# Kernel tuning notes

Hardware: AMD Instinct MI355X
Metric: run time of the kernel (lower is better)

Reference implementation:

```python
import jax, jax.numpy as jnp
import numpy as np

T = 2048          # tokens (single-sequence prefill)
HID = 4096        # hidden_size
NH = 32           # num attention heads
NKV = 8           # num kv heads (GQA)
HD = 128          # head_dim
QKV_OUT = (NH + 2 * NKV) * HD  # 6144
THETA = 10000.0
SCALING = HD ** -0.5


def setup_inputs() -> dict:
    key = jax.random.key(0)
    ks = jax.random.split(key, 8)
    positions = jnp.arange(T, dtype=jnp.int32)
    # per-token int8 quantized hidden states (symmetric, [-127,127])
    q_act = jax.random.randint(ks[0], (T, HID), -127, 128, dtype=jnp.int32)
    # per-token dynamic activation scale
    act_scale = jax.random.uniform(ks[1], (T,), jnp.float32) * 0.01 + 0.001
    # int4 weights stored unsigned [0,15] with per-output-channel scale & zero point
    w_qkv_q = jax.random.randint(ks[2], (QKV_OUT, HID), 0, 16, dtype=jnp.int32)
    w_qkv_scale = jax.random.uniform(ks[3], (QKV_OUT,), jnp.float32) * 0.01 + 0.001
    w_qkv_zero = jax.random.uniform(ks[4], (QKV_OUT,), jnp.float32) * 2.0 + 7.0
    w_o_q = jax.random.randint(ks[5], (HID, HID), 0, 16, dtype=jnp.int32)
    w_o_scale = jax.random.uniform(ks[6], (HID,), jnp.float32) * 0.01 + 0.001
    w_o_zero = jax.random.uniform(ks[7], (HID,), jnp.float32) * 2.0 + 7.0
    return dict(positions=positions, q_act=q_act, act_scale=act_scale,
                w_qkv_q=w_qkv_q, w_qkv_scale=w_qkv_scale, w_qkv_zero=w_qkv_zero,
                w_o_q=w_o_q, w_o_scale=w_o_scale, w_o_zero=w_o_zero)


def w4a8_linear(qa_f, s_a, a_sum, qw, s_w, z_w):
    # y[t,o] = s_a[t]*s_w[o] * ( (qa @ qw^T)[t,o] - z_w[o]*sum_j qa[t,j] )
    acc = jnp.matmul(qa_f, qw.astype(jnp.float32).T)  # [T, O]
    return (s_a[:, None] * s_w[None, :]) * (acc - z_w[None, :] * a_sum[:, None])


def apply_rope(x, positions):
    # neox-style RoPE over full head_dim
    half = HD // 2
    inv_freq = THETA ** (-jnp.arange(0, half, dtype=jnp.float32) / half * 1.0)
    inv_freq = 1.0 / (THETA ** (jnp.arange(0, HD, 2, dtype=jnp.float32) / HD))
    freqs = positions.astype(jnp.float32)[:, None] * inv_freq[None, :]  # [T, HD/2]
    cos = jnp.cos(freqs)[:, None, :]
    sin = jnp.sin(freqs)[:, None, :]
    x1, x2 = x[..., :half], x[..., half:]
    return jnp.concatenate([x1 * cos - x2 * sin, x2 * cos + x1 * sin], axis=-1)


def dynamic_quant_with_sum(x):
    # per-token symmetric int8 dynamic quantization + fused sum
    s = jnp.maximum(jnp.max(jnp.abs(x), axis=-1), 1e-8) / 127.0  # [T]
    q = jnp.clip(jnp.round(x / s[:, None]), -127, 127)
    return q, s, jnp.sum(q, axis=-1)


def reference(positions, q_act, act_scale, w_qkv_q, w_qkv_scale, w_qkv_zero,
              w_o_q, w_o_scale, w_o_zero):
    qa_f = q_act.astype(jnp.float32)
    a_sum = jnp.sum(qa_f, axis=-1)  # fused activation sum
    qkv = w4a8_linear(qa_f, act_scale, a_sum, w_qkv_q, w_qkv_scale, w_qkv_zero)
    q, k, v = jnp.split(qkv, [NH * HD, NH * HD + NKV * HD], axis=-1)
    q = q.reshape(T, NH, HD)
    k = k.reshape(T, NKV, HD)
    v = v.reshape(T, NKV, HD)
    q = apply_rope(q, positions)
    k = apply_rope(k, positions)
    # GQA: repeat kv heads
    rep = NH // NKV
    k = jnp.repeat(k, rep, axis=1)  # [T, NH, HD]
    v = jnp.repeat(v, rep, axis=1)
    scores = jnp.einsum('qhd,khd->hqk', q, k) * SCALING  # [NH, T, T]
    causal = jnp.tril(jnp.ones((T, T), dtype=bool))
    scores = jnp.where(causal[None], scores, -jnp.inf)
    probs = jax.nn.softmax(scores, axis=-1)
    attn = jnp.einsum('hqk,khd->qhd', probs, v).reshape(T, NH * HD)
    # invoke_quant_fuse_sum: dynamic per-token quantization of attn output
    q2, s2, sum2 = dynamic_quant_with_sum(attn)
    out = w4a8_linear(q2, s2, sum2, w_o_q, w_o_scale, w_o_zero)
    return out
```

## Files before the change

### kernel.cpp

```cpp
#include <hip/hip_runtime.h>

#define T 2048
#define HID 4096
#define NH 32
#define NKV 8
#define HD 128
#define QKV_OUT ((NH + 2*NKV) * HD)
#define SCALING 0.08838834764831843f
#define ROPE_C 0.20762050593046014f

typedef __attribute__((ext_vector_type(8))) short bfrag;
typedef __attribute__((ext_vector_type(4))) float ffrag;
typedef __attribute__((ext_vector_type(4))) int  ifrag;
typedef __attribute__((ext_vector_type(16))) char c16;

__device__ __forceinline__ short f2bf(float f) {
  unsigned u = __builtin_bit_cast(unsigned, f);
  u += 0x7fffu + ((u >> 16) & 1u);
  return (short)(u >> 16);
}

__device__ __forceinline__ void split2(float x, short& hi, short& lo) {
  unsigned u = __builtin_bit_cast(unsigned, x);
  unsigned uh = u + (0x7fffu + ((u >> 16) & 1u));
  hi = (short)(uh >> 16);
  float fh = __builtin_bit_cast(float, uh & 0xffff0000u);
  float r = x - fh;
  unsigned ur = __builtin_bit_cast(unsigned, r);
  ur += 0x7fffu + ((ur >> 16) & 1u);
  lo = (short)(ur >> 16);
}

__device__ __forceinline__ void gload_lds16(const void* g, void* l) {
  __builtin_amdgcn_global_load_lds(
      (const __attribute__((address_space(1))) unsigned int*)g,
      (__attribute__((address_space(3))) unsigned int*)l, 16, 0, 0);
}

__global__ __launch_bounds__(256)
void asum_conv(const int* __restrict__ qact, float* __restrict__ a_sum,
               char* __restrict__ a_i8) {
  __shared__ int red[256];
  const int t = blockIdx.x, tid = threadIdx.x;
  const int* row = qact + (size_t)t * HID + tid * 16;
  int s = 0;
  c16 o;
#pragma unroll
  for (int i = 0; i < 4; i++) {
    int4 v = *(const int4*)(row + i * 4);
    s += v.x + v.y + v.z + v.w;
    o[i*4+0] = (char)v.x; o[i*4+1] = (char)v.y;
    o[i*4+2] = (char)v.z; o[i*4+3] = (char)v.w;
  }
  *(c16*)(a_i8 + (size_t)t * HID + tid * 16) = o;
  red[tid] = s; __syncthreads();
  for (int off = 128; off > 0; off >>= 1) {
    if (tid < off) red[tid] += red[tid + off];
    __syncthreads();
  }
  if (tid == 0) a_sum[t] = (float)red[0];
}

__global__ __launch_bounds__(256)
void conv_i2c(const int* __restrict__ src, char* __restrict__ dst, int n16) {
  int idx = blockIdx.x * 256 + threadIdx.x;
  if (idx >= n16) return;
  const int4* s4 = (const int4*)src + (size_t)idx * 4;
  c16 o;
#pragma unroll
  for (int j = 0; j < 4; j++) {
    int4 v = s4[j];
    o[j*4+0] = (char)v.x; o[j*4+1] = (char)v.y;
    o[j*4+2] = (char)v.z; o[j*4+3] = (char)v.w;
  }
  *(c16*)(dst + (size_t)idx * 16) = o;
}

__global__ __launch_bounds__(256)
void gemm_i8(const char* __restrict__ A, const char* __restrict__ W,
             const float* __restrict__ s_a, const float* __restrict__ asum,
             const float* __restrict__ s_w, const float* __restrict__ z_w,
             float* __restrict__ C, int M, int N, int K) {
  __shared__ __align__(16) char As[128 * 64];
  __shared__ __align__(16) char Bs[128 * 64];
  const int tid = threadIdx.x;
  const int lane = tid & 63;
  const int quad = lane >> 4, l15 = lane & 15;
  const int wave = tid >> 6;
  const int wm = (wave >> 1) * 64, wn = (wave & 1) * 64;
  const int bm = blockIdx.y * 128, bn = blockIdx.x * 128;
  const int sr = tid >> 2, sc = (tid & 3) * 16;

  ifrag acc[4][4];
#pragma unroll
  for (int mi = 0; mi < 4; mi++)
#pragma unroll
    for (int ni = 0; ni < 4; ni++)
      acc[mi][ni] = (ifrag){0, 0, 0, 0};

  for (int k0 = 0; k0 < K; k0 += 64) {
#pragma unroll
    for (int it = 0; it < 2; it++) {
      gload_lds16(A + (size_t)(bm + it * 64 + sr) * K + k0 + sc,
                  &As[it * 4096 + wave * 1024]);
      gload_lds16(W + (size_t)(bn + it * 64 + sr) * K + k0 + sc,
                  &Bs[it * 4096 + wave * 1024]);
    }
    __syncthreads();

    ifrag af[4], bfv[4];
#pragma unroll
    for (int mi = 0; mi < 4; mi++)
      af[mi] = *(const ifrag*)&As[(wm + mi * 16 + l15) * 64 + quad * 16];
#pragma unroll
    for (int ni = 0; ni < 4; ni++)
      bfv[ni] = *(const ifrag*)&Bs[(wn + ni * 16 + l15) * 64 + quad * 16];
#pragma unroll
    for (int mi = 0; mi < 4; mi++)
#pragma unroll
      for (int ni = 0; ni < 4; ni++)
        acc[mi][ni] = __builtin_amdgcn_mfma_i32_16x16x64_i8(
            af[mi], bfv[ni], acc[mi][ni], 0, 0, 0);
    __syncthreads();
  }

#pragma unroll
  for (int mi = 0; mi < 4; mi++) {
    int row0 = bm + wm + mi * 16 + quad * 4;
#pragma unroll
    for (int r = 0; r < 4; r++) {
      int row = row0 + r;
      float sa = s_a[row], av = asum[row];
#pragma unroll
      for (int ni = 0; ni < 4; ni++) {
        int col = bn + wn + ni * 16 + l15;
        C[(size_t)row * N + col] = (sa * s_w[col]) * ((float)acc[mi][ni][r] - z_w[col] * av);
      }
    }
  }
}

__global__ __launch_bounds__(256)
void split_kv(float* __restrict__ qkv, const int* __restrict__ positions,
              short* __restrict__ Kh, short* __restrict__ Kl,
              short* __restrict__ Vth) {
  __shared__ __align__(16) short Vh_lds[128 * 72];
  const int y = blockIdx.y;
  const int t0 = blockIdx.x * 64;
  const int tid = threadIdx.x;

  if (y >= NKV) {
    const int h = y - NKV;
#pragma unroll
    for (int it = 0; it < 4; it++) {
      int c = tid + 256 * it;
      int key = c >> 4, dc = c & 15;
      float* qr = qkv + (size_t)(t0 + key) * QKV_OUT + (size_t)h * HD;
      float4 a = *(const float4*)(qr + dc * 4);
      float4 b = *(const float4*)(qr + dc * 4 + 64);
      float av[4] = {a.x, a.y, a.z, a.w};
      float bv[4] = {b.x, b.y, b.z, b.w};
      float pos = (float)positions[t0 + key];
#pragma unroll
      for (int jj = 0; jj < 4; jj++) {
        float fr = pos * exp2f(-ROPE_C * (float)(dc * 4 + jj));
        float sn, cs; sincosf(fr, &sn, &cs);
        float x1 = av[jj], x2 = bv[jj];
        av[jj] = x1 * cs - x2 * sn;
        bv[jj] = x2 * cs + x1 * sn;
      }
      *(float4*)(qr + dc * 4)      = make_float4(av[0], av[1], av[2], av[3]);
      *(float4*)(qr + dc * 4 + 64) = make_float4(bv[0], bv[1], bv[2], bv[3]);
    }
    return;
  }

  const int kvh = y;
#pragma unroll
  for (int it = 0; it < 4; it++) {
    int c = tid + 256 * it;
    int key = c >> 4, dc = c & 15;
    const float* kr = qkv + (size_t)(t0 + key) * QKV_OUT
                      + (size_t)NH * HD + (size_t)kvh * HD;
    float4 a = *(const float4*)(kr + dc * 4);
    float4 b = *(const float4*)(kr + dc * 4 + 64);
    float av[4] = {a.x, a.y, a.z, a.w};
    float bv[4] = {b.x, b.y, b.z, b.w};
    float pos = (float)positions[t0 + key];
    short4 ha, la, hb, lb;
    short hh, ll;
#pragma unroll
    for (int jj = 0; jj < 4; jj++) {
      float fr = pos * exp2f(-ROPE_C * (float)(dc * 4 + jj));
      float sn, cs; sincosf(fr, &sn, &cs);
      float x1 = av[jj], x2 = bv[jj];
      float r1 = x1 * cs - x2 * sn;
      float r2 = x2 * cs + x1 * sn;
      split2(r1, hh, ll); ((short*)&ha)[jj] = hh; ((short*)&la)[jj] = ll;
      split2(r2, hh, ll); ((short*)&hb)[jj] = hh; ((short*)&lb)[jj] = ll;
    }
    size_t o1 = (size_t)kvh * T * HD + (size_t)(t0 + key) * HD + dc * 4;
    *(short4*)(Kh + o1) = ha;      *(short4*)(Kl + o1) = la;
    *(short4*)(Kh + o1 + 64) = hb; *(short4*)(Kl + o1 + 64) = lb;
  }
#pragma unroll
  for (int i = 0; i < 8; i++) {
    int c = tid + 256 * i;
    int key = c >> 5, dc = c & 31;
    float4 f = *(const float4*)(qkv + (size_t)(t0 + key) * QKV_OUT
                                + (size_t)(NH + NKV) * HD + (size_t)kvh * HD + dc * 4);
    Vh_lds[(dc*4+0)*72 + key] = f2bf(f.x);
    Vh_lds[(dc*4+1)*72 + key] = f2bf(f.y);
    Vh_lds[(dc*4+2)*72 + key] = f2bf(f.z);
    Vh_lds[(dc*4+3)*72 + key] = f2bf(f.w);
  }
  __syncthreads();
#pragma unroll
  for (int i = 0; i < 2; i++) {
    int c = tid + 256 * i;
    int row = c >> 2, cc = c & 3;
    size_t o = (size_t)kvh * HD * T + (size_t)row * T + t0 + cc * 8;
    *(bfrag*)(Vth + o) = *(const bfrag*)&Vh_lds[row * 72 + cc * 8];
  }
#pragma unroll
  for (int i = 0; i < 2; i++) {
    int c = tid + 256 * i;
    int row = c >> 2, cc = c & 3;
    size_t o = (size_t)kvh * HD * T + (size_t)row * T + t0 + 32 + cc * 8;
    *(bfrag*)(Vth + o) = *(const bfrag*)&Vh_lds[row * 72 + 32 + cc * 8];
  }
}

__global__ __launch_bounds__(256)
void attn_kernel(const float* __restrict__ qkv,
                 const short* __restrict__ Kh, const short* __restrict__ Kl,
                 const short* __restrict__ Vth,
                 float* __restrict__ attn) {
  __shared__ __align__(16) short Ksh[32 * 136];
  __shared__ __align__(16) short Ksl[32 * 136];
  __shared__ __align__(16) short Vsh[128 * 40];
  __shared__ __align__(16) short Psh[4 * 16 * 40];

  const int kvh = blockIdx.y;
  const int pair = blockIdx.x;
  const int tid = threadIdx.x;
  const int lane = tid & 63;
  const int wv = tid >> 6;
  const int l15 = lane & 15, quad = lane >> 4;
  const int h = kvh * 4 + wv;
  short* Pw = Psh + wv * 16 * 40;

  const short* KhB = Kh + (size_t)kvh * T * HD;
  const short* KlB = Kl + (size_t)kvh * T * HD;
  const short* VhB = Vth + (size_t)kvh * HD * T;

  const int kr = tid >> 4, kc8 = (tid & 15) * 8;
  const int vd = tid >> 2, vc8 = (tid & 3) * 8;

  bfrag rkh0, rkh1, rkl0, rkl1, rv0, rv1;
  auto preload = [&](int k0) {
    rkh0 = *(const bfrag*)(KhB + (size_t)(k0 + kr) * HD + kc8);
    rkh1 = *(const bfrag*)(KhB + (size_t)(k0 + kr + 16) * HD + kc8);
    rkl0 = *(const bfrag*)(KlB + (size_t)(k0 + kr) * HD + kc8);
    rkl1 = *(const bfrag*)(KlB + (size_t)(k0 + kr + 16) * HD + kc8);
    rv0  = *(const bfrag*)(VhB + (size_t)vd * T + k0 + vc8);
    rv1  = *(const bfrag*)(VhB + (size_t)(vd + 64) * T + k0 + vc8);
  };
  preload(0);

  bfrag ones;
#pragma unroll
  for (int j = 0; j < 8; j++) ones[j] = (short)0x3f80;

  for (int pass = 0; pass < 2; pass++) {
    const int qt = pass ? pair : 127 - pair;
    const int q0 = qt * 16;
    const int nk = (q0 >> 5) + 1;

    bfrag qh[4], ql[4];
    const float* qrow = qkv + (size_t)(q0 + l15) * QKV_OUT + (size_t)h * HD;
#pragma unroll
    for (int kc = 0; kc < 4; kc++) {
      float4 f0 = *(const float4*)(qrow + kc * 32 + quad * 8);
      float4 f1 = *(const float4*)(qrow + kc * 32 + quad * 8 + 4);
      float fv[8] = {f0.x, f0.y, f0.z, f0.w, f1.x, f1.y, f1.z, f1.w};
#pragma unroll
      for (int j = 0; j < 8; j++) {
        short hi, lo; split2(fv[j], hi, lo);
        qh[kc][j] = hi; ql[kc][j] = lo;
      }
    }

    ffrag o[8], ol;
    ol = (ffrag){0.f, 0.f, 0.f, 0.f};
#pragma unroll
    for (int n = 0; n < 8; n++) o[n] = (ffrag){0.f, 0.f, 0.f, 0.f};
    float m_i[4] = {-1e30f, -1e30f, -1e30f, -1e30f};

    for (int kt = 0; kt < nk; kt++) {
      const int k0 = kt << 5;
      __syncthreads();
      *(bfrag*)&Ksh[kr * 136 + kc8] = rkh0;
      *(bfrag*)&Ksh[(kr + 16) * 136 + kc8] = rkh1;
      *(bfrag*)&Ksl[kr * 136 + kc8] = rkl0;
      *(bfrag*)&Ksl[(kr + 16) * 136 + kc8] = rkl1;
      *(bfrag*)&Vsh[vd * 40 + vc8] = rv0;
      *(bfrag*)&Vsh[(vd + 64) * 40 + vc8] = rv1;
      if (kt + 1 < nk) preload(k0 + 32);
      else if (pass == 0) preload(0);
      __syncthreads();

      ffrag s[2];
      s[0] = (ffrag){0.f,0.f,0.f,0.f}; s[1] = (ffrag){0.f,0.f,0.f,0.f};
#pragma unroll
      for (int n = 0; n < 2; n++) {
#pragma unroll
        for (int kc = 0; kc < 4; kc++) {
          bfrag bh = *(const bfrag*)&Ksh[(n*16 + l15) * 136 + kc*32 + quad*8];
          bfrag bl = *(const bfrag*)&Ksl[(n*16 + l15) * 136 + kc*32 + quad*8];
          s[n] = __builtin_amdgcn_mfma_f32_16x16x32_bf16(qh[kc], bh, s[n], 0,0,0);
          s[n] = __builtin_amdgcn_mfma_f32_16x16x32_bf16(qh[kc], bl, s[n], 0,0,0);
          s[n] = __builtin_amdgcn_mfma_f32_16x16x32_bf16(ql[kc], bh, s[n], 0,0,0);
        }
      }
      const bool last = (kt == nk - 1);
      float sv[2][4];
#pragma unroll
      for (int n = 0; n < 2; n++)
#pragma unroll
        for (int r = 0; r < 4; r++) {
          float v = s[n][r] * SCALING;
          if (last) {
            int key = k0 + n * 16 + l15;
            int row = q0 + quad * 4 + r;
            if (key > row) v = -1e30f;
          }
          sv[n][r] = v;
        }
      float alpha[4];
      bool anyup = false;
#pragma unroll
      for (int r = 0; r < 4; r++) {
        float mt = fmaxf(sv[0][r], sv[1][r]);
        mt = fmaxf(mt, __shfl_xor(mt, 1));
        mt = fmaxf(mt, __shfl_xor(mt, 2));
        mt = fmaxf(mt, __shfl_xor(mt, 4));
        mt = fmaxf(mt, __shfl_xor(mt, 8));
        float m_new = fmaxf(m_i[r], mt);
        alpha[r] = __expf(m_i[r] - m_new);
        if (m_new > m_i[r]) anyup = true;
        m_i[r] = m_new;
      }
#pragma unroll
      for (int n = 0; n < 2; n++)
#pragma unroll
        for (int r = 0; r < 4; r++) {
          float p = __expf(sv[n][r] - m_i[r]);
          Pw[(quad*4 + r) * 40 + n*16 + l15] = f2bf(p);
        }
      if (__any(anyup)) {
#pragma unroll
        for (int r = 0; r < 4; r++) ol[r] *= alpha[r];
#pragma unroll
        for (int n = 0; n < 8; n++)
#pragma unroll
          for (int r = 0; r < 4; r++) o[n][r] *= alpha[r];
      }
      bfrag ph = *(const bfrag*)&Pw[l15 * 40 + quad * 8];
      ol = __builtin_amdgcn_mfma_f32_16x16x32_bf16(ph, ones, ol, 0,0,0);
#pragma unroll
      for (int n = 0; n < 8; n++) {
        bfrag vh = *(const bfrag*)&Vsh[(n*16 + l15) * 40 + quad * 8];
        o[n] = __builtin_amdgcn_mfma_f32_16x16x32_bf16(ph, vh, o[n], 0,0,0);
      }
    }

    float inv[4];
#pragma unroll
    for (int r = 0; r < 4; r++) inv[r] = 1.f / ol[r];
#pragma unroll
    for (int n = 0; n < 8; n++)
#pragma unroll
      for (int r = 0; r < 4; r++) {
        int row = q0 + quad * 4 + r;
        attn[(size_t)row * HID + (size_t)h * HD + n * 16 + l15] = o[n][r] * inv[r];
      }
  }
}

__global__ __launch_bounds__(256)
void quant_kernel(const float* __restrict__ x, char* __restrict__ q2,
                  float* __restrict__ s2, float* __restrict__ sum2) {
  __shared__ float red[256];
  const int t = blockIdx.x, tid = threadIdx.x;
  const float* row = x + (size_t)t * HID;
  float4 v[4];
  float m = 0.f;
#pragma unroll
  for (int i = 0; i < 4; i++) {
    v[i] = *(const float4*)(row + tid * 16 + i * 4);
    m = fmaxf(m, fmaxf(fmaxf(fabsf(v[i].x), fabsf(v[i].y)),
                       fmaxf(fabsf(v[i].z), fabsf(v[i].w))));
  }
  red[tid] = m; __syncthreads();
  for (int off = 128; off > 0; off >>= 1) {
    if (tid < off) red[tid] = fmaxf(red[tid], red[tid + off]);
    __syncthreads();
  }
  float s = fmaxf(red[0], 1e-8f) / 127.f;
  __syncthreads();
  float ssum = 0.f;
  c16 o;
#pragma unroll
  for (int i = 0; i < 4; i++) {
    float q;
    q = fminf(127.f, fmaxf(-127.f, rintf(v[i].x / s))); ssum += q; o[i*4+0] = (char)(int)q;
    q = fminf(127.f, fmaxf(-127.f, rintf(v[i].y / s))); ssum += q; o[i*4+1] = (char)(int)q;
    q = fminf(127.f, fmaxf(-127.f, rintf(v[i].z / s))); ssum += q; o[i*4+2] = (char)(int)q;
    q = fminf(127.f, fmaxf(-127.f, rintf(v[i].w / s))); ssum += q; o[i*4+3] = (char)(int)q;
  }
  *(c16*)(q2 + (size_t)t * HID + tid * 16) = o;
  red[tid] = ssum; __syncthreads();
  for (int off = 128; off > 0; off >>= 1) {
    if (tid < off) red[tid] += red[tid + off];
    __syncthreads();
  }
  if (tid == 0) { s2[t] = s; sum2[t] = red[0]; }
}

extern "C" void kernel_launch(void* const* d_in, const int* in_sizes, int n_in,
                              void* d_out, int out_size, void* d_ws, size_t ws_size,
                              hipStream_t stream) {
  const int*   positions   = (const int*)d_in[0];
  const int*   q_act       = (const int*)d_in[1];
  const float* act_scale   = (const float*)d_in[2];
  const int*   w_qkv_q     = (const int*)d_in[3];
  const float* w_qkv_scale = (const float*)d_in[4];
  const float* w_qkv_zero  = (const float*)d_in[5];
  const int*   w_o_q       = (const int*)d_in[6];
  const float* w_o_scale   = (const float*)d_in[7];
  const float* w_o_zero    = (const float*)d_in[8];
  float* out = (float*)d_out;

  size_t off = 0;
  auto alloc = [&](size_t bytes) -> void* {
    void* p = (char*)d_ws + off;
    off += (bytes + 255) & ~(size_t)255;
    return p;
  };
  float* qkv   = (float*)alloc((size_t)T * QKV_OUT * 4);
  char*  act8  = (char*)alloc((size_t)T * HID);
  short* Kh    = (short*)alloc((size_t)NKV * T * HD * 2);
  short* Kl    = (short*)alloc((size_t)NKV * T * HD * 2);
  short* Vth   = (short*)alloc((size_t)NKV * T * HD * 2);
  char*  w8    = (char*)alloc((size_t)QKV_OUT * HID);
  float* a_sum = (float*)alloc(T * 4);
  float* s2    = (float*)alloc(T * 4);
  float* sum2  = (float*)alloc(T * 4);
  (void)ws_size;

  asum_conv<<<T, 256, 0, stream>>>(q_act, a_sum, act8);
  conv_i2c<<<(QKV_OUT * HID / 16 + 255) / 256, 256, 0, stream>>>(
      w_qkv_q, w8, QKV_OUT * HID / 16);
  gemm_i8<<<dim3(QKV_OUT / 128, T / 128), 256, 0, stream>>>(
      act8, w8, act_scale, a_sum, w_qkv_scale, w_qkv_zero, qkv, T, QKV_OUT, HID);
  split_kv<<<dim3(T / 64, NKV + NH), 256, 0, stream>>>(qkv, positions, Kh, Kl, Vth);
  attn_kernel<<<dim3(64, NKV), 256, 0, stream>>>(qkv, Kh, Kl, Vth, out);
  conv_i2c<<<(HID * HID / 16 + 255) / 256, 256, 0, stream>>>(
      w_o_q, w8, HID * HID / 16);
  quant_kernel<<<T, 256, 0, stream>>>(out, act8, s2, sum2);
  gemm_i8<<<dim3(HID / 128, T / 128), 256, 0, stream>>>(
      act8, w8, s2, sum2, w_o_scale, w_o_zero, out, T, HID, HID);
}
```

Measured before the change: 535.2 us.

## Split attention KV range across two blocks and merge partials in a combine kernel

Each (query-tile pair, kv head) block is split into two blocks, one for even and one for odd 32-key tiles. This doubles the attention grid to improve CU occupancy and load balance. Each half writes unnormalised outputs plus its running max and sum. A new combine kernel rescales the two halves with log-sum-exp weights and writes the normalised result. The partial buffer reuses the act8/w8 workspace region, and launch bounds now request 4 waves per EU. The cost is an extra kernel launch and roughly two extra full passes over the fp32 attention output in memory.

Result: slower. 758.4 us (+41.7%).

```diff
diff --git a/kernel.cpp b/kernel.cpp
--- a/kernel.cpp
+++ b/kernel.cpp
@@ -231,18 +231,20 @@
   }
 }
 
-__global__ __launch_bounds__(256)
+__global__ __launch_bounds__(256, 4)
 void attn_kernel(const float* __restrict__ qkv,
                  const short* __restrict__ Kh, const short* __restrict__ Kl,
                  const short* __restrict__ Vth,
-                 float* __restrict__ attn) {
+                 float* __restrict__ Opart, float* __restrict__ Mp,
+                 float* __restrict__ Lp, float* __restrict__ attn) {
   __shared__ __align__(16) short Ksh[32 * 136];
   __shared__ __align__(16) short Ksl[32 * 136];
   __shared__ __align__(16) short Vsh[128 * 40];
   __shared__ __align__(16) short Psh[4 * 16 * 40];
 
   const int kvh = blockIdx.y;
-  const int pair = blockIdx.x;
+  const int pair = blockIdx.x >> 1;
+  const int half = blockIdx.x & 1;
   const int tid = threadIdx.x;
   const int lane = tid & 63;
   const int wv = tid >> 6;
@@ -266,7 +268,7 @@
     rv0  = *(const bfrag*)(VhB + (size_t)vd * T + k0 + vc8);
     rv1  = *(const bfrag*)(VhB + (size_t)(vd + 64) * T + k0 + vc8);
   };
-  preload(0);
+  preload(half * 32);
 
   bfrag ones;
 #pragma unroll
@@ -297,7 +299,7 @@
     for (int n = 0; n < 8; n++) o[n] = (ffrag){0.f, 0.f, 0.f, 0.f};
     float m_i[4] = {-1e30f, -1e30f, -1e30f, -1e30f};
 
-    for (int kt = 0; kt < nk; kt++) {
+    for (int kt = half; kt < nk; kt += 2) {
       const int k0 = kt << 5;
       __syncthreads();
       *(bfrag*)&Ksh[kr * 136 + kc8] = rkh0;
@@ -306,8 +308,8 @@
       *(bfrag*)&Ksl[(kr + 16) * 136 + kc8] = rkl1;
       *(bfrag*)&Vsh[vd * 40 + vc8] = rv0;
       *(bfrag*)&Vsh[(vd + 64) * 40 + vc8] = rv1;
-      if (kt + 1 < nk) preload(k0 + 32);
-      else if (pass == 0) preload(0);
+      if (kt + 2 < nk) preload(k0 + 64);
+      else if (pass == 0) preload(half * 32);
       __syncthreads();
 
       ffrag s[2];
@@ -375,16 +377,48 @@
       }
     }
 
-    float inv[4];
-#pragma unroll
-    for (int r = 0; r < 4; r++) inv[r] = 1.f / ol[r];
+    float* dst = half ? attn : Opart;
 #pragma unroll
     for (int n = 0; n < 8; n++)
 #pragma unroll
       for (int r = 0; r < 4; r++) {
         int row = q0 + quad * 4 + r;
-        attn[(size_t)row * HID + (size_t)h * HD + n * 16 + l15] = o[n][r] * inv[r];
-      }
+        dst[(size_t)row * HID + (size_t)h * HD + n * 16 + l15] = o[n][r];
+      }
+    if (l15 == 0) {
+#pragma unroll
+      for (int r = 0; r < 4; r++) {
+        int row = q0 + quad * 4 + r;
+        size_t ix = (size_t)half * NH * T + (size_t)h * T + row;
+        Mp[ix] = m_i[r];
+        Lp[ix] = ol[r];
+      }
+    }
+  }
+}
+
+__global__ __launch_bounds__(256)
+void attn_combine(const float* __restrict__ Opart, const float* __restrict__ Mp,
+                  const float* __restrict__ Lp, float* attn) {
+  const int row = blockIdx.x, tid = threadIdx.x;
+  const int h = tid >> 3;
+  const float m0 = Mp[(size_t)h * T + row];
+  const float m1 = Mp[(size_t)NH * T + (size_t)h * T + row];
+  const float l0 = Lp[(size_t)h * T + row];
+  const float l1 = Lp[(size_t)NH * T + (size_t)h * T + row];
+  const float m = fmaxf(m0, m1);
+  float s0 = __expf(m0 - m), s1 = __expf(m1 - m);
+  const float inv = 1.f / (l0 * s0 + l1 * s1);
+  s0 *= inv; s1 *= inv;
+  const size_t base = (size_t)row * HID + (size_t)tid * 16;
+  float4* dst = (float4*)(attn + base);
+  const float4* p0 = (const float4*)(Opart + base);
+#pragma unroll
+  for (int i = 0; i < 4; i++) {
+    float4 a = p0[i];
+    float4 b = dst[i];
+    dst[i] = make_float4(a.x * s0 + b.x * s1, a.y * s0 + b.y * s1,
+                         a.z * s0 + b.z * s1, a.w * s0 + b.w * s1);
   }
 }
 
@@ -450,13 +484,16 @@
   };
   float* qkv   = (float*)alloc((size_t)T * QKV_OUT * 4);
   char*  act8  = (char*)alloc((size_t)T * HID);
+  char*  w8    = (char*)alloc((size_t)QKV_OUT * HID);
   short* Kh    = (short*)alloc((size_t)NKV * T * HD * 2);
   short* Kl    = (short*)alloc((size_t)NKV * T * HD * 2);
   short* Vth   = (short*)alloc((size_t)NKV * T * HD * 2);
-  char*  w8    = (char*)alloc((size_t)QKV_OUT * HID);
   float* a_sum = (float*)alloc(T * 4);
   float* s2    = (float*)alloc(T * 4);
   float* sum2  = (float*)alloc(T * 4);
+  float* Mp    = (float*)alloc((size_t)2 * NH * T * 4);
+  float* Lp    = (float*)alloc((size_t)2 * NH * T * 4);
+  float* Opart = (float*)act8;
   (void)ws_size;
 
   asum_conv<<<T, 256, 0, stream>>>(q_act, a_sum, act8);
@@ -465,7 +502,9 @@
   gemm_i8<<<dim3(QKV_OUT / 128, T / 128), 256, 0, stream>>>(
       act8, w8, act_scale, a_sum, w_qkv_scale, w_qkv_zero, qkv, T, QKV_OUT, HID);
   split_kv<<<dim3(T / 64, NKV + NH), 256, 0, stream>>>(qkv, positions, Kh, Kl, Vth);
-  attn_kernel<<<dim3(64, NKV), 256, 0, stream>>>(qkv, Kh, Kl, Vth, out);
+  attn_kernel<<<dim3(128, NKV), 256, 0, stream>>>(
+      qkv, Kh, Kl, Vth, Opart, Mp, Lp, out);
+  attn_combine<<<T, 256, 0, stream>>>(Opart, Mp, Lp, out);
   conv_i2c<<<(HID * HID / 16 + 255) / 256, 256, 0, stream>>>(
       w_o_q, w8, HID * HID / 16);
   quant_kernel<<<T, 256, 0, stream>>>(out, act8, s2, sum2);
```
